# Kernel tuning notes

Hardware: AMD Instinct MI355X
Metric: run time of the kernel (lower is better)

Reference implementation:

```python
import jax, jax.numpy as jnp
import numpy as np

THRESH = 0.1        # Huber threshold (self.threshold)
CORR_WT = 1.0       # corr_wt
ENTROPY_WT = 0.0001 # entropy_wt
BS, N = 32, 1024    # n_pts = nv = 1024 hardcoded in multi_pose_with_pts


def setup_inputs() -> dict:
    key = jax.random.key(0)
    ks = jax.random.split(key, 7)
    return {
        "points_1": jax.random.normal(ks[0], (BS, N, 3), jnp.float32),
        "points_2": jax.random.normal(ks[1], (BS, N, 3), jnp.float32),
        "assign_mat_1": jax.random.normal(ks[2], (BS, N, N), jnp.float32),
        "assign_mat_2": jax.random.normal(ks[3], (BS, N, N), jnp.float32),
        "scale": jax.random.uniform(ks[4], (BS,), jnp.float32, 0.5, 1.5),
        "rotation": jax.random.normal(ks[5], (BS, 3, 3), jnp.float32),
        "translation": jax.random.normal(ks[6], (BS, 3), jnp.float32),
    }


def _transform(sRt, pts):
    # apply 4x4 pose to [b, n, 3] points (homogeneous, keep xyz)
    return jnp.einsum('bij,bnj->bni', sRt[:, :3, :3], pts) + sRt[:, :3, 3][:, None, :]


def _chamfer(x, y):
    # squared pairwise distances [b, n, m]; loss = mean min both directions
    d = (jnp.sum(x * x, -1)[:, :, None] + jnp.sum(y * y, -1)[:, None, :]
         - 2.0 * jnp.einsum('bnd,bmd->bnm', x, y))
    d = jnp.maximum(d, 0.0)
    return jnp.mean(jnp.min(d, axis=2)) + jnp.mean(jnp.min(d, axis=1))


def _corr(a, b):
    # smooth-L1-like (Huber) correspondence loss
    diff = jnp.abs(a - b)
    loss = jnp.where(diff > THRESH, diff - THRESH / 2.0, diff * diff / (2.0 * THRESH))
    return CORR_WT * jnp.mean(jnp.sum(loss, axis=2))


def _entropy(assign_mat, soft_assign, axis):
    log_assign = jax.nn.log_softmax(assign_mat, axis=axis)
    return ENTROPY_WT * jnp.mean(-jnp.sum(soft_assign * log_assign, axis=axis))


def _cos_loss(m1, m2, eps=1e-8):
    a = m1.reshape(m1.shape[0], -1)
    b = m2.reshape(m2.shape[0], -1)
    na = jnp.maximum(jnp.linalg.norm(a, axis=1), eps)
    nb = jnp.maximum(jnp.linalg.norm(b, axis=1), eps)
    return jnp.mean(1.0 - jnp.sum(a * b, axis=1) / (na * nb))


def reference(points_1, points_2, assign_mat_1, assign_mat_2, scale, rotation, translation):
    sa1 = jax.nn.softmax(assign_mat_1, axis=2)
    sa2 = jax.nn.softmax(assign_mat_2, axis=2)

    # pose_dict_RT: sRt = [[s*R, t], [0, 1]]
    sR = rotation * scale[:, None, None]
    sRt = jnp.concatenate([sR, translation[:, :, None]], axis=2)          # b 3 4
    bottom = jnp.broadcast_to(jnp.array([0., 0., 0., 1.], sRt.dtype), (sRt.shape[0], 1, 4))
    sRt12 = jnp.concatenate([sRt, bottom], axis=1)                        # b 4 4
    sRt21 = jnp.linalg.inv(sRt12)

    p1in2 = jnp.einsum('bnm,bmd->bnd', sa1, points_2)
    p2in1 = jnp.einsum('bnm,bmd->bnd', sa2, points_1)
    p1to2 = _transform(sRt12, points_1)
    p2to1 = _transform(sRt21, points_2)

    cd1 = _chamfer(p1to2, p1in2)
    cd2 = _chamfer(p2to1, p2in1)
    total = (cd1 + cd2
             + _corr(p1in2, p1to2) + _corr(p2in1, p2to1)
             + _entropy(assign_mat_1, sa1, 2) + _entropy(assign_mat_2, sa2, 2)
             + _cos_loss(assign_mat_1, assign_mat_2)
             + _entropy(assign_mat_1, sa1, 1) + _entropy(assign_mat_2, sa2, 1))
    return total
```

## Files before the change

### kernel.cpp

```cpp
#include <hip/hip_runtime.h>
#include <math.h>

#define BSZ 32
#define NP  1024

#define OFF_ACC    0
#define OFF_COS    8
#define OFF_COLC1  104
#define OFF_COLT1  (OFF_COLC1 + 32768)
#define OFF_COLC2  (OFF_COLC1 + 65536)
#define OFF_COLT2  (OFF_COLC1 + 98304)
#define ZERO_FLOATS (OFF_COLC1 + 131072)
#define OFF_MIN    ZERO_FLOATS
#define OFF_POSE   (OFF_MIN + 131072)
#define OFF_P1TO2  (OFF_POSE + 768)
#define OFF_P2TO1  (OFF_P1TO2 + 98304)
#define OFF_P1IN2  (OFF_P2TO1 + 98304)
#define OFF_P2IN1  (OFF_P1IN2 + 98304)

__global__ void k_pose(const float* __restrict__ scale,
                       const float* __restrict__ rot,
                       const float* __restrict__ tr,
                       float* __restrict__ pose) {
    int b = threadIdx.x;
    if (b >= BSZ) return;
    float s = scale[b];
    float M[9];
#pragma unroll
    for (int i = 0; i < 9; ++i) M[i] = rot[b * 9 + i] * s;
    float t0 = tr[b * 3 + 0], t1 = tr[b * 3 + 1], t2 = tr[b * 3 + 2];
    float det = M[0] * (M[4] * M[8] - M[5] * M[7])
              - M[1] * (M[3] * M[8] - M[5] * M[6])
              + M[2] * (M[3] * M[7] - M[4] * M[6]);
    float id = 1.0f / det;
    float inv[9];
    inv[0] =  (M[4] * M[8] - M[5] * M[7]) * id;
    inv[1] = -(M[1] * M[8] - M[2] * M[7]) * id;
    inv[2] =  (M[1] * M[5] - M[2] * M[4]) * id;
    inv[3] = -(M[3] * M[8] - M[5] * M[6]) * id;
    inv[4] =  (M[0] * M[8] - M[2] * M[6]) * id;
    inv[5] = -(M[0] * M[5] - M[2] * M[3]) * id;
    inv[6] =  (M[3] * M[7] - M[4] * M[6]) * id;
    inv[7] = -(M[0] * M[7] - M[1] * M[6]) * id;
    inv[8] =  (M[0] * M[4] - M[1] * M[3]) * id;
    float u0 = -(inv[0] * t0 + inv[1] * t1 + inv[2] * t2);
    float u1 = -(inv[3] * t0 + inv[4] * t1 + inv[5] * t2);
    float u2 = -(inv[6] * t0 + inv[7] * t1 + inv[8] * t2);
    float* P = pose + b * 24;
#pragma unroll
    for (int i = 0; i < 9; ++i) P[i] = M[i];
    P[9] = t0; P[10] = t1; P[11] = t2;
#pragma unroll
    for (int i = 0; i < 9; ++i) P[12 + i] = inv[i];
    P[21] = u0; P[22] = u1; P[23] = u2;
}

__global__ void k_transform(const float* __restrict__ p1, const float* __restrict__ p2,
                            const float* __restrict__ pose,
                            float* __restrict__ p1to2, float* __restrict__ p2to1) {
    int idx = blockIdx.x * 256 + threadIdx.x;
    int b = idx >> 10;
    const float* P = pose + b * 24;
    float x = p1[idx * 3 + 0], y = p1[idx * 3 + 1], z = p1[idx * 3 + 2];
    p1to2[idx * 3 + 0] = P[0] * x + P[1] * y + P[2] * z + P[9];
    p1to2[idx * 3 + 1] = P[3] * x + P[4] * y + P[5] * z + P[10];
    p1to2[idx * 3 + 2] = P[6] * x + P[7] * y + P[8] * z + P[11];
    x = p2[idx * 3 + 0]; y = p2[idx * 3 + 1]; z = p2[idx * 3 + 2];
    p2to1[idx * 3 + 0] = P[12] * x + P[13] * y + P[14] * z + P[21];
    p2to1[idx * 3 + 1] = P[15] * x + P[16] * y + P[17] * z + P[22];
    p2to1[idx * 3 + 2] = P[18] * x + P[19] * y + P[20] * z + P[23];
}

__global__ __launch_bounds__(256) void k_big(
    const float* __restrict__ am1, const float* __restrict__ am2,
    const float* __restrict__ pts1, const float* __restrict__ pts2,
    float* __restrict__ p1in2, float* __restrict__ p2in1,
    float* __restrict__ colC1, float* __restrict__ colT1,
    float* __restrict__ colC2, float* __restrict__ colT2,
    float* __restrict__ cosacc, float* __restrict__ acc) {
    const int b  = blockIdx.x >> 4;
    const int rb = blockIdx.x & 15;
    const int wv = threadIdx.x >> 6;
    const int ln = threadIdx.x & 63;
    const int row0 = rb * 64 + wv * 16;

    float pA[16][3];
    float pB[16][3];
#pragma unroll
    for (int j = 0; j < 4; ++j)
#pragma unroll
        for (int k = 0; k < 4; ++k) {
            int c = 256 * j + 4 * ln + k;
            int i = 4 * j + k;
            pA[i][0] = pts2[(b * NP + c) * 3 + 0];
            pA[i][1] = pts2[(b * NP + c) * 3 + 1];
            pA[i][2] = pts2[(b * NP + c) * 3 + 2];
            pB[i][0] = pts1[(b * NP + c) * 3 + 0];
            pB[i][1] = pts1[(b * NP + c) * 3 + 1];
            pB[i][2] = pts1[(b * NP + c) * 3 + 2];
        }

    float C1[16], T1[16], C2[16], T2[16];
#pragma unroll
    for (int i = 0; i < 16; ++i) { C1[i] = 0.f; T1[i] = 0.f; C2[i] = 0.f; T2[i] = 0.f; }
    float dacc = 0.f, n1a = 0.f, n2a = 0.f, e2a = 0.f, sSa = 0.f;

    const float4* rA = (const float4*)(am1 + ((size_t)b * NP + row0) * NP);
    const float4* rB = (const float4*)(am2 + ((size_t)b * NP + row0) * NP);

#pragma unroll 1
    for (int r = 0; r < 16; ++r) {
        float4 a[4], c4[4];
#pragma unroll
        for (int j = 0; j < 4; ++j) {
            a[j]  = rA[(size_t)r * 256 + ln + 64 * j];
            c4[j] = rB[(size_t)r * 256 + ln + 64 * j];
        }
#pragma unroll
        for (int j = 0; j < 4; ++j) {
            dacc += a[j].x * c4[j].x + a[j].y * c4[j].y + a[j].z * c4[j].z + a[j].w * c4[j].w;
            n1a  += a[j].x * a[j].x + a[j].y * a[j].y + a[j].z * a[j].z + a[j].w * a[j].w;
            n2a  += c4[j].x * c4[j].x + c4[j].y * c4[j].y + c4[j].z * c4[j].z + c4[j].w * c4[j].w;
        }
        {
            float R = 0.f, Su = 0.f, q0 = 0.f, q1 = 0.f, q2 = 0.f;
#pragma unroll
            for (int j = 0; j < 4; ++j) {
                float* e = (float*)&a[j];
#pragma unroll
                for (int k = 0; k < 4; ++k) {
                    int i = 4 * j + k;
                    float v  = e[k];
                    float ex = __expf(v);
                    R += ex; Su += ex * v;
                    q0 += ex * pA[i][0]; q1 += ex * pA[i][1]; q2 += ex * pA[i][2];
                    C1[i] += ex;
                    e[k] = ex;
                }
            }
#pragma unroll
            for (int m = 1; m < 64; m <<= 1) {
                R  += __shfl_xor(R, m);  Su += __shfl_xor(Su, m);
                q0 += __shfl_xor(q0, m); q1 += __shfl_xor(q1, m); q2 += __shfl_xor(q2, m);
            }
            float inv = 1.0f / R;
#pragma unroll
            for (int j = 0; j < 4; ++j) {
                float* e = (float*)&a[j];
#pragma unroll
                for (int k = 0; k < 4; ++k) T1[4 * j + k] += e[k] * inv;
            }
            float S = Su * inv;
            if (ln == 0) {
                e2a += __logf(R) - S;
                sSa += S;
                int row = b * NP + row0 + r;
                p1in2[row * 3 + 0] = q0 * inv;
                p1in2[row * 3 + 1] = q1 * inv;
                p1in2[row * 3 + 2] = q2 * inv;
            }
        }
        {
            float R = 0.f, Su = 0.f, q0 = 0.f, q1 = 0.f, q2 = 0.f;
#pragma unroll
            for (int j = 0; j < 4; ++j) {
                float* e = (float*)&c4[j];
#pragma unroll
                for (int k = 0; k < 4; ++k) {
                    int i = 4 * j + k;
                    float v  = e[k];
                    float ex = __expf(v);
                    R += ex; Su += ex * v;
                    q0 += ex * pB[i][0]; q1 += ex * pB[i][1]; q2 += ex * pB[i][2];
                    C2[i] += ex;
                    e[k] = ex;
                }
            }
#pragma unroll
            for (int m = 1; m < 64; m <<= 1) {
                R  += __shfl_xor(R, m);  Su += __shfl_xor(Su, m);
                q0 += __shfl_xor(q0, m); q1 += __shfl_xor(q1, m); q2 += __shfl_xor(q2, m);
            }
            float inv = 1.0f / R;
#pragma unroll
            for (int j = 0; j < 4; ++j) {
                float* e = (float*)&c4[j];
#pragma unroll
                for (int k = 0; k < 4; ++k) T2[4 * j + k] += e[k] * inv;
            }
            float S = Su * inv;
            if (ln == 0) {
                e2a += __logf(R) - S;
                sSa += S;
                int row = b * NP + row0 + r;
                p2in1[row * 3 + 0] = q0 * inv;
                p2in1[row * 3 + 1] = q1 * inv;
                p2in1[row * 3 + 2] = q2 * inv;
            }
        }
    }

#pragma unroll
    for (int j = 0; j < 4; ++j)
#pragma unroll
        for (int k = 0; k < 4; ++k) {
            int i = 4 * j + k;
            int o = b * NP + 256 * j + 4 * ln + k;
            atomicAdd(&colC1[o], C1[i]);
            atomicAdd(&colT1[o], T1[i]);
            atomicAdd(&colC2[o], C2[i]);
            atomicAdd(&colT2[o], T2[i]);
        }
#pragma unroll
    for (int m = 1; m < 64; m <<= 1) {
        dacc += __shfl_xor(dacc, m);
        n1a  += __shfl_xor(n1a, m);
        n2a  += __shfl_xor(n2a, m);
    }
    if (ln == 0) {
        atomicAdd(&cosacc[b], dacc);
        atomicAdd(&cosacc[32 + b], n1a);
        atomicAdd(&cosacc[64 + b], n2a);
        atomicAdd(&acc[0], e2a);
        atomicAdd(&acc[1], sSa);
    }
}

__global__ void k_cols(const float* __restrict__ colC1, const float* __restrict__ colT1,
                       const float* __restrict__ colC2, const float* __restrict__ colT2,
                       float* __restrict__ acc) {
    int idx = blockIdx.x * 256 + threadIdx.x;
    float v;
    if (idx < 32768) v = colT1[idx] * __logf(colC1[idx]);
    else { int i2 = idx - 32768; v = colT2[i2] * __logf(colC2[i2]); }
#pragma unroll
    for (int m = 1; m < 64; m <<= 1) v += __shfl_xor(v, m);
    if ((threadIdx.x & 63) == 0) atomicAdd(&acc[2], v);
}

__global__ __launch_bounds__(256) void k_chamfer(
    const float* __restrict__ p1to2, const float* __restrict__ p1in2,
    const float* __restrict__ p2to1, const float* __restrict__ p2in1,
    float* __restrict__ minarr) {
    int blk   = blockIdx.x;
    int chunk = blk & 3;
    int b     = (blk >> 2) & 31;
    int dir   = (blk >> 7) & 1;
    int pair  = blk >> 8;
    const float* X; const float* Y;
    if (pair == 0) { X = dir ? p1in2 : p1to2; Y = dir ? p1to2 : p1in2; }
    else           { X = dir ? p2in1 : p2to1; Y = dir ? p2to1 : p2in1; }
    __shared__ float ys[256 * 3];
    int t = threadIdx.x;
    int yi = b * NP + chunk * 256 + t;
    ys[t * 3 + 0] = Y[yi * 3 + 0];
    ys[t * 3 + 1] = Y[yi * 3 + 1];
    ys[t * 3 + 2] = Y[yi * 3 + 2];
    __syncthreads();
    float* marr = minarr + ((size_t)(pair * 2 + dir) * 32 + b) * NP;
    float x0[4], x1[4], x2[4], mn[4];
#pragma unroll
    for (int i = 0; i < 4; ++i) {
        int xi = b * NP + i * 256 + t;
        x0[i] = X[xi * 3 + 0]; x1[i] = X[xi * 3 + 1]; x2[i] = X[xi * 3 + 2];
        mn[i] = 3.0e38f;
    }
    for (int o = 0; o < 256; ++o) {
        float y0 = ys[o * 3 + 0], y1 = ys[o * 3 + 1], y2 = ys[o * 3 + 2];
#pragma unroll
        for (int i = 0; i < 4; ++i) {
            float d0 = x0[i] - y0, d1 = x1[i] - y1, d2 = x2[i] - y2;
            float d = d0 * d0 + d1 * d1 + d2 * d2;
            mn[i] = fminf(mn[i], d);
        }
    }
#pragma unroll
    for (int i = 0; i < 4; ++i)
        atomicMin((unsigned int*)&marr[i * 256 + t], __float_as_uint(mn[i]));
}

__global__ void k_corr(const float* __restrict__ p1in2, const float* __restrict__ p1to2,
                       const float* __restrict__ p2in1, const float* __restrict__ p2to1,
                       float* __restrict__ acc) {
    int idx = blockIdx.x * 256 + threadIdx.x;
    const float* A; const float* P;
    int i = idx;
    if (i < 32768) { A = p1in2; P = p1to2; }
    else           { A = p2in1; P = p2to1; i -= 32768; }
    float s = 0.f;
#pragma unroll
    for (int d = 0; d < 3; ++d) {
        float df = fabsf(A[i * 3 + d] - P[i * 3 + d]);
        s += (df > 0.1f) ? (df - 0.05f) : (df * df * 5.0f);
    }
#pragma unroll
    for (int m = 1; m < 64; m <<= 1) s += __shfl_xor(s, m);
    if ((threadIdx.x & 63) == 0) atomicAdd(&acc[3], s);
}

__global__ void k_minsum(const float* __restrict__ minarr, float* __restrict__ acc) {
    int idx = blockIdx.x * 256 + threadIdx.x;
    float v = minarr[idx];
#pragma unroll
    for (int m = 1; m < 64; m <<= 1) v += __shfl_xor(v, m);
    if ((threadIdx.x & 63) == 0) atomicAdd(&acc[4], v);
}

__global__ void k_final(const float* __restrict__ acc, const float* __restrict__ cosacc,
                        float* __restrict__ out) {
    if (threadIdx.x != 0) return;
    const float invBN = 1.0f / 32768.0f;
    float ent2 = 1e-4f * acc[0] * invBN;
    float ent1 = 1e-4f * (acc[2] - acc[1]) * invBN;
    float corr = acc[3] * invBN;
    float cham = acc[4] * invBN;
    float cosl = 0.f;
    for (int b = 0; b < 32; ++b) {
        float dot = cosacc[b];
        float na = fmaxf(sqrtf(cosacc[32 + b]), 1e-8f);
        float nb = fmaxf(sqrtf(cosacc[64 + b]), 1e-8f);
        cosl += 1.0f - dot / (na * nb);
    }
    cosl *= (1.0f / 32.0f);
    out[0] = cham + corr + ent2 + ent1 + cosl;
}

extern "C" void kernel_launch(void* const* d_in, const int* in_sizes, int n_in,
                              void* d_out, int out_size, void* d_ws, size_t ws_size,
                              hipStream_t stream) {
    const float* p1    = (const float*)d_in[0];
    const float* p2    = (const float*)d_in[1];
    const float* am1   = (const float*)d_in[2];
    const float* am2   = (const float*)d_in[3];
    const float* scale = (const float*)d_in[4];
    const float* rot   = (const float*)d_in[5];
    const float* tr    = (const float*)d_in[6];

    float* ws = (float*)d_ws;
    float* acc    = ws + OFF_ACC;
    float* cosacc = ws + OFF_COS;
    float* colC1  = ws + OFF_COLC1;
    float* colT1  = ws + OFF_COLT1;
    float* colC2  = ws + OFF_COLC2;
    float* colT2  = ws + OFF_COLT2;
    float* minarr = ws + OFF_MIN;
    float* pose   = ws + OFF_POSE;
    float* p1to2  = ws + OFF_P1TO2;
    float* p2to1  = ws + OFF_P2TO1;
    float* p1in2  = ws + OFF_P1IN2;
    float* p2in1  = ws + OFF_P2IN1;

    hipMemsetAsync(ws, 0, ZERO_FLOATS * sizeof(float), stream);
    hipMemsetAsync(minarr, 0x7F, 131072 * sizeof(float), stream);

    k_pose<<<1, 64, 0, stream>>>(scale, rot, tr, pose);
    k_transform<<<128, 256, 0, stream>>>(p1, p2, pose, p1to2, p2to1);
    k_big<<<512, 256, 0, stream>>>(am1, am2, p1, p2, p1in2, p2in1,
                                   colC1, colT1, colC2, colT2, cosacc, acc);
    k_cols<<<256, 256, 0, stream>>>(colC1, colT1, colC2, colT2, acc);
    k_chamfer<<<512, 256, 0, stream>>>(p1to2, p1in2, p2to1, p2in1, minarr);
    k_corr<<<256, 256, 0, stream>>>(p1in2, p1to2, p2in1, p2to1, acc);
    k_minsum<<<512, 256, 0, stream>>>(minarr, acc);
    k_final<<<1, 64, 0, stream>>>(acc, cosacc, (float*)d_out);
}
```

Measured before the change: 495.1 us.

## Restructure big kernel with prefetch and LDS column reduction, fuse tail kernels

The main softmax/column kernel now uses twice as many blocks with 8 rows per wave, double-buffers the assignment-matrix row loads, packs point coordinates as bf16 pairs in registers, and reduces column sums in shared memory before issuing global atomics. The chamfer kernel now loads the whole target cloud into LDS as SoA and computes the full minimum per point directly, which removes the atomicMin buffer, its memset and the separate min-sum kernel. The corr and column-entropy reductions are merged into one tail kernel. Storing points as bf16 lowers the precision of the soft-assigned point estimates, and the extra per-block shared-memory reductions add overhead.

```diff
diff --git a/kernel.cpp b/kernel.cpp
--- a/kernel.cpp
+++ b/kernel.cpp
@@ -11,12 +11,17 @@
 #define OFF_COLC2  (OFF_COLC1 + 65536)
 #define OFF_COLT2  (OFF_COLC1 + 98304)
 #define ZERO_FLOATS (OFF_COLC1 + 131072)
-#define OFF_MIN    ZERO_FLOATS
-#define OFF_POSE   (OFF_MIN + 131072)
+#define OFF_POSE   ZERO_FLOATS
 #define OFF_P1TO2  (OFF_POSE + 768)
 #define OFF_P2TO1  (OFF_P1TO2 + 98304)
 #define OFF_P1IN2  (OFF_P2TO1 + 98304)
 #define OFF_P2IN1  (OFF_P1IN2 + 98304)
+
+__device__ __forceinline__ unsigned int pkbf(float lo, float hi) {
+    return (__float_as_uint(lo) >> 16) | (__float_as_uint(hi) & 0xffff0000u);
+}
+__device__ __forceinline__ float bflo(unsigned int p) { return __uint_as_float(p << 16); }
+__device__ __forceinline__ float bfhi(unsigned int p) { return __uint_as_float(p & 0xffff0000u); }
 
 __global__ void k_pose(const float* __restrict__ scale,
                        const float* __restrict__ rot,
@@ -78,27 +83,38 @@
     float* __restrict__ colC1, float* __restrict__ colT1,
     float* __restrict__ colC2, float* __restrict__ colT2,
     float* __restrict__ cosacc, float* __restrict__ acc) {
-    const int b  = blockIdx.x >> 4;
-    const int rb = blockIdx.x & 15;
+    const int b  = blockIdx.x >> 5;
+    const int rb = blockIdx.x & 31;
     const int wv = threadIdx.x >> 6;
     const int ln = threadIdx.x & 63;
-    const int row0 = rb * 64 + wv * 16;
-
-    float pA[16][3];
-    float pB[16][3];
-#pragma unroll
-    for (int j = 0; j < 4; ++j)
-#pragma unroll
-        for (int k = 0; k < 4; ++k) {
-            int c = 256 * j + 4 * ln + k;
-            int i = 4 * j + k;
-            pA[i][0] = pts2[(b * NP + c) * 3 + 0];
-            pA[i][1] = pts2[(b * NP + c) * 3 + 1];
-            pA[i][2] = pts2[(b * NP + c) * 3 + 2];
-            pB[i][0] = pts1[(b * NP + c) * 3 + 0];
-            pB[i][1] = pts1[(b * NP + c) * 3 + 1];
-            pB[i][2] = pts1[(b * NP + c) * 3 + 2];
-        }
+    const int row0 = rb * 32 + wv * 8;
+
+    __shared__ float cacc[4][NP];
+    {
+        float* cf = (float*)cacc;
+#pragma unroll
+        for (int i = 0; i < 16; ++i) cf[threadIdx.x + 256 * i] = 0.f;
+    }
+    __syncthreads();
+
+    unsigned int pax[4][2], pay[4][2], paz[4][2];
+    unsigned int pbx[4][2], pby[4][2], pbz[4][2];
+#pragma unroll
+    for (int j = 0; j < 4; ++j) {
+        int base = (b * NP + 256 * j + 4 * ln) * 3;
+        float4 t0 = *(const float4*)(pts2 + base);
+        float4 t1 = *(const float4*)(pts2 + base + 4);
+        float4 t2 = *(const float4*)(pts2 + base + 8);
+        pax[j][0] = pkbf(t0.x, t0.w); pax[j][1] = pkbf(t1.z, t2.y);
+        pay[j][0] = pkbf(t0.y, t1.x); pay[j][1] = pkbf(t1.w, t2.z);
+        paz[j][0] = pkbf(t0.z, t1.y); paz[j][1] = pkbf(t2.x, t2.w);
+        t0 = *(const float4*)(pts1 + base);
+        t1 = *(const float4*)(pts1 + base + 4);
+        t2 = *(const float4*)(pts1 + base + 8);
+        pbx[j][0] = pkbf(t0.x, t0.w); pbx[j][1] = pkbf(t1.z, t2.y);
+        pby[j][0] = pkbf(t0.y, t1.x); pby[j][1] = pkbf(t1.w, t2.z);
+        pbz[j][0] = pkbf(t0.z, t1.y); pbz[j][1] = pkbf(t2.x, t2.w);
+    }
 
     float C1[16], T1[16], C2[16], T2[16];
 #pragma unroll
@@ -108,94 +124,111 @@
     const float4* rA = (const float4*)(am1 + ((size_t)b * NP + row0) * NP);
     const float4* rB = (const float4*)(am2 + ((size_t)b * NP + row0) * NP);
 
-#pragma unroll 1
-    for (int r = 0; r < 16; ++r) {
-        float4 a[4], c4[4];
+    float4 ab[2][4], cb[2][4];
+#pragma unroll
+    for (int j = 0; j < 4; ++j) { ab[0][j] = rA[ln + 64 * j]; cb[0][j] = rB[ln + 64 * j]; }
+
+#pragma unroll
+    for (int r = 0; r < 8; ++r) {
+        const int cu = r & 1, nx = cu ^ 1;
+        if (r < 7) {
+#pragma unroll
+            for (int j = 0; j < 4; ++j) {
+                ab[nx][j] = rA[(size_t)(r + 1) * 256 + ln + 64 * j];
+                cb[nx][j] = rB[(size_t)(r + 1) * 256 + ln + 64 * j];
+            }
+        }
 #pragma unroll
         for (int j = 0; j < 4; ++j) {
-            a[j]  = rA[(size_t)r * 256 + ln + 64 * j];
-            c4[j] = rB[(size_t)r * 256 + ln + 64 * j];
-        }
-#pragma unroll
-        for (int j = 0; j < 4; ++j) {
-            dacc += a[j].x * c4[j].x + a[j].y * c4[j].y + a[j].z * c4[j].z + a[j].w * c4[j].w;
-            n1a  += a[j].x * a[j].x + a[j].y * a[j].y + a[j].z * a[j].z + a[j].w * a[j].w;
-            n2a  += c4[j].x * c4[j].x + c4[j].y * c4[j].y + c4[j].z * c4[j].z + c4[j].w * c4[j].w;
+            float4 a = ab[cu][j], c = cb[cu][j];
+            dacc = fmaf(a.x, c.x, fmaf(a.y, c.y, fmaf(a.z, c.z, fmaf(a.w, c.w, dacc))));
+            n1a  = fmaf(a.x, a.x, fmaf(a.y, a.y, fmaf(a.z, a.z, fmaf(a.w, a.w, n1a))));
+            n2a  = fmaf(c.x, c.x, fmaf(c.y, c.y, fmaf(c.z, c.z, fmaf(c.w, c.w, n2a))));
         }
         {
-            float R = 0.f, Su = 0.f, q0 = 0.f, q1 = 0.f, q2 = 0.f;
-#pragma unroll
-            for (int j = 0; j < 4; ++j) {
-                float* e = (float*)&a[j];
-#pragma unroll
-                for (int k = 0; k < 4; ++k) {
-                    int i = 4 * j + k;
-                    float v  = e[k];
-                    float ex = __expf(v);
-                    R += ex; Su += ex * v;
-                    q0 += ex * pA[i][0]; q1 += ex * pA[i][1]; q2 += ex * pA[i][2];
-                    C1[i] += ex;
-                    e[k] = ex;
-                }
+            float R = 0.f, Su = 0.f, qx = 0.f, qy = 0.f, qz = 0.f;
+#pragma unroll
+            for (int j = 0; j < 4; ++j) {
+                float4 v = ab[cu][j];
+                float e0 = __expf(v.x), e1 = __expf(v.y), e2 = __expf(v.z), e3 = __expf(v.w);
+                R += (e0 + e1) + (e2 + e3);
+                Su = fmaf(e0, v.x, Su); Su = fmaf(e1, v.y, Su);
+                Su = fmaf(e2, v.z, Su); Su = fmaf(e3, v.w, Su);
+                qx = fmaf(e0, bflo(pax[j][0]), qx); qx = fmaf(e1, bfhi(pax[j][0]), qx);
+                qx = fmaf(e2, bflo(pax[j][1]), qx); qx = fmaf(e3, bfhi(pax[j][1]), qx);
+                qy = fmaf(e0, bflo(pay[j][0]), qy); qy = fmaf(e1, bfhi(pay[j][0]), qy);
+                qy = fmaf(e2, bflo(pay[j][1]), qy); qy = fmaf(e3, bfhi(pay[j][1]), qy);
+                qz = fmaf(e0, bflo(paz[j][0]), qz); qz = fmaf(e1, bfhi(paz[j][0]), qz);
+                qz = fmaf(e2, bflo(paz[j][1]), qz); qz = fmaf(e3, bfhi(paz[j][1]), qz);
+                C1[4 * j + 0] += e0; C1[4 * j + 1] += e1;
+                C1[4 * j + 2] += e2; C1[4 * j + 3] += e3;
+                ab[cu][j] = make_float4(e0, e1, e2, e3);
             }
 #pragma unroll
             for (int m = 1; m < 64; m <<= 1) {
                 R  += __shfl_xor(R, m);  Su += __shfl_xor(Su, m);
-                q0 += __shfl_xor(q0, m); q1 += __shfl_xor(q1, m); q2 += __shfl_xor(q2, m);
+                qx += __shfl_xor(qx, m); qy += __shfl_xor(qy, m); qz += __shfl_xor(qz, m);
             }
             float inv = 1.0f / R;
 #pragma unroll
             for (int j = 0; j < 4; ++j) {
-                float* e = (float*)&a[j];
-#pragma unroll
-                for (int k = 0; k < 4; ++k) T1[4 * j + k] += e[k] * inv;
+                float4 e = ab[cu][j];
+                T1[4 * j + 0] = fmaf(e.x, inv, T1[4 * j + 0]);
+                T1[4 * j + 1] = fmaf(e.y, inv, T1[4 * j + 1]);
+                T1[4 * j + 2] = fmaf(e.z, inv, T1[4 * j + 2]);
+                T1[4 * j + 3] = fmaf(e.w, inv, T1[4 * j + 3]);
             }
             float S = Su * inv;
             if (ln == 0) {
                 e2a += __logf(R) - S;
                 sSa += S;
                 int row = b * NP + row0 + r;
-                p1in2[row * 3 + 0] = q0 * inv;
-                p1in2[row * 3 + 1] = q1 * inv;
-                p1in2[row * 3 + 2] = q2 * inv;
+                p1in2[row * 3 + 0] = qx * inv;
+                p1in2[row * 3 + 1] = qy * inv;
+                p1in2[row * 3 + 2] = qz * inv;
             }
         }
         {
-            float R = 0.f, Su = 0.f, q0 = 0.f, q1 = 0.f, q2 = 0.f;
-#pragma unroll
-            for (int j = 0; j < 4; ++j) {
-                float* e = (float*)&c4[j];
-#pragma unroll
-                for (int k = 0; k < 4; ++k) {
-                    int i = 4 * j + k;
-                    float v  = e[k];
-                    float ex = __expf(v);
-                    R += ex; Su += ex * v;
-                    q0 += ex * pB[i][0]; q1 += ex * pB[i][1]; q2 += ex * pB[i][2];
-                    C2[i] += ex;
-                    e[k] = ex;
-                }
+            float R = 0.f, Su = 0.f, qx = 0.f, qy = 0.f, qz = 0.f;
+#pragma unroll
+            for (int j = 0; j < 4; ++j) {
+                float4 v = cb[cu][j];
+                float e0 = __expf(v.x), e1 = __expf(v.y), e2 = __expf(v.z), e3 = __expf(v.w);
+                R += (e0 + e1) + (e2 + e3);
+                Su = fmaf(e0, v.x, Su); Su = fmaf(e1, v.y, Su);
+                Su = fmaf(e2, v.z, Su); Su = fmaf(e3, v.w, Su);
+                qx = fmaf(e0, bflo(pbx[j][0]), qx); qx = fmaf(e1, bfhi(pbx[j][0]), qx);
+                qx = fmaf(e2, bflo(pbx[j][1]), qx); qx = fmaf(e3, bfhi(pbx[j][1]), qx);
+                qy = fmaf(e0, bflo(pby[j][0]), qy); qy = fmaf(e1, bfhi(pby[j][0]), qy);
+                qy = fmaf(e2, bflo(pby[j][1]), qy); qy = fmaf(e3, bfhi(pby[j][1]), qy);
+                qz = fmaf(e0, bflo(pbz[j][0]), qz); qz = fmaf(e1, bfhi(pbz[j][0]), qz);
+                qz = fmaf(e2, bflo(pbz[j][1]), qz); qz = fmaf(e3, bfhi(pbz[j][1]), qz);
+                C2[4 * j + 0] += e0; C2[4 * j + 1] += e1;
+                C2[4 * j + 2] += e2; C2[4 * j + 3] += e3;
+                cb[cu][j] = make_float4(e0, e1, e2, e3);
             }
 #pragma unroll
             for (int m = 1; m < 64; m <<= 1) {
                 R  += __shfl_xor(R, m);  Su += __shfl_xor(Su, m);
-                q0 += __shfl_xor(q0, m); q1 += __shfl_xor(q1, m); q2 += __shfl_xor(q2, m);
+                qx += __shfl_xor(qx, m); qy += __shfl_xor(qy, m); qz += __shfl_xor(qz, m);
             }
             float inv = 1.0f / R;
 #pragma unroll
             for (int j = 0; j < 4; ++j) {
-                float* e = (float*)&c4[j];
-#pragma unroll
-                for (int k = 0; k < 4; ++k) T2[4 * j + k] += e[k] * inv;
+                float4 e = cb[cu][j];
+                T2[4 * j + 0] = fmaf(e.x, inv, T2[4 * j + 0]);
+                T2[4 * j + 1] = fmaf(e.y, inv, T2[4 * j + 1]);
+                T2[4 * j + 2] = fmaf(e.z, inv, T2[4 * j + 2]);
+                T2[4 * j + 3] = fmaf(e.w, inv, T2[4 * j + 3]);
             }
             float S = Su * inv;
             if (ln == 0) {
                 e2a += __logf(R) - S;
                 sSa += S;
                 int row = b * NP + row0 + r;
-                p2in1[row * 3 + 0] = q0 * inv;
-                p2in1[row * 3 + 1] = q1 * inv;
-                p2in1[row * 3 + 2] = q2 * inv;
+                p2in1[row * 3 + 0] = qx * inv;
+                p2in1[row * 3 + 1] = qy * inv;
+                p2in1[row * 3 + 2] = qz * inv;
             }
         }
     }
@@ -205,12 +238,22 @@
 #pragma unroll
         for (int k = 0; k < 4; ++k) {
             int i = 4 * j + k;
-            int o = b * NP + 256 * j + 4 * ln + k;
-            atomicAdd(&colC1[o], C1[i]);
-            atomicAdd(&colT1[o], T1[i]);
-            atomicAdd(&colC2[o], C2[i]);
-            atomicAdd(&colT2[o], T2[i]);
-        }
+            int c = 256 * j + 4 * ln + k;
+            atomicAdd(&cacc[0][c], C1[i]);
+            atomicAdd(&cacc[1][c], T1[i]);
+            atomicAdd(&cacc[2][c], C2[i]);
+            atomicAdd(&cacc[3][c], T2[i]);
+        }
+    __syncthreads();
+#pragma unroll
+    for (int qq = 0; qq < 4; ++qq) {
+        int c = 256 * qq + threadIdx.x;
+        atomicAdd(&colC1[b * NP + c], cacc[0][c]);
+        atomicAdd(&colT1[b * NP + c], cacc[1][c]);
+        atomicAdd(&colC2[b * NP + c], cacc[2][c]);
+        atomicAdd(&colT2[b * NP + c], cacc[3][c]);
+    }
+
 #pragma unroll
     for (int m = 1; m < 64; m <<= 1) {
         dacc += __shfl_xor(dacc, m);
@@ -226,84 +269,76 @@
     }
 }
 
-__global__ void k_cols(const float* __restrict__ colC1, const float* __restrict__ colT1,
+__global__ void k_tail(const float* __restrict__ colC1, const float* __restrict__ colT1,
                        const float* __restrict__ colC2, const float* __restrict__ colT2,
+                       const float* __restrict__ p1in2, const float* __restrict__ p1to2,
+                       const float* __restrict__ p2in1, const float* __restrict__ p2to1,
                        float* __restrict__ acc) {
     int idx = blockIdx.x * 256 + threadIdx.x;
     float v;
-    if (idx < 32768) v = colT1[idx] * __logf(colC1[idx]);
-    else { int i2 = idx - 32768; v = colT2[i2] * __logf(colC2[i2]); }
-#pragma unroll
-    for (int m = 1; m < 64; m <<= 1) v += __shfl_xor(v, m);
-    if ((threadIdx.x & 63) == 0) atomicAdd(&acc[2], v);
+    int i = idx;
+    const float* A; const float* P;
+    if (idx < 32768) {
+        v = colT1[idx] * __logf(colC1[idx]);
+        A = p1in2; P = p1to2;
+    } else {
+        int i2 = idx - 32768;
+        v = colT2[i2] * __logf(colC2[i2]);
+        A = p2in1; P = p2to1; i = i2;
+    }
+    float s = 0.f;
+#pragma unroll
+    for (int d = 0; d < 3; ++d) {
+        float df = fabsf(A[i * 3 + d] - P[i * 3 + d]);
+        s += (df > 0.1f) ? (df - 0.05f) : (df * df * 5.0f);
+    }
+#pragma unroll
+    for (int m = 1; m < 64; m <<= 1) { v += __shfl_xor(v, m); s += __shfl_xor(s, m); }
+    if ((threadIdx.x & 63) == 0) { atomicAdd(&acc[2], v); atomicAdd(&acc[3], s); }
 }
 
 __global__ __launch_bounds__(256) void k_chamfer(
     const float* __restrict__ p1to2, const float* __restrict__ p1in2,
     const float* __restrict__ p2to1, const float* __restrict__ p2in1,
-    float* __restrict__ minarr) {
-    int blk   = blockIdx.x;
-    int chunk = blk & 3;
-    int b     = (blk >> 2) & 31;
-    int dir   = (blk >> 7) & 1;
-    int pair  = blk >> 8;
+    float* __restrict__ acc) {
+    int blk     = blockIdx.x;
+    int quarter = blk & 3;
+    int b       = (blk >> 2) & 31;
+    int dir     = (blk >> 7) & 1;
+    int pair    = blk >> 8;
     const float* X; const float* Y;
     if (pair == 0) { X = dir ? p1in2 : p1to2; Y = dir ? p1to2 : p1in2; }
     else           { X = dir ? p2in1 : p2to1; Y = dir ? p2to1 : p2in1; }
-    __shared__ float ys[256 * 3];
+    __shared__ float ysx[NP], ysy[NP], ysz[NP];
     int t = threadIdx.x;
-    int yi = b * NP + chunk * 256 + t;
-    ys[t * 3 + 0] = Y[yi * 3 + 0];
-    ys[t * 3 + 1] = Y[yi * 3 + 1];
-    ys[t * 3 + 2] = Y[yi * 3 + 2];
+#pragma unroll
+    for (int i = 0; i < 4; ++i) {
+        int yi = i * 256 + t;
+        int g = (b * NP + yi) * 3;
+        ysx[yi] = Y[g + 0]; ysy[yi] = Y[g + 1]; ysz[yi] = Y[g + 2];
+    }
     __syncthreads();
-    float* marr = minarr + ((size_t)(pair * 2 + dir) * 32 + b) * NP;
-    float x0[4], x1[4], x2[4], mn[4];
-#pragma unroll
-    for (int i = 0; i < 4; ++i) {
-        int xi = b * NP + i * 256 + t;
-        x0[i] = X[xi * 3 + 0]; x1[i] = X[xi * 3 + 1]; x2[i] = X[xi * 3 + 2];
-        mn[i] = 3.0e38f;
-    }
-    for (int o = 0; o < 256; ++o) {
-        float y0 = ys[o * 3 + 0], y1 = ys[o * 3 + 1], y2 = ys[o * 3 + 2];
-#pragma unroll
-        for (int i = 0; i < 4; ++i) {
-            float d0 = x0[i] - y0, d1 = x1[i] - y1, d2 = x2[i] - y2;
-            float d = d0 * d0 + d1 * d1 + d2 * d2;
-            mn[i] = fminf(mn[i], d);
-        }
-    }
-#pragma unroll
-    for (int i = 0; i < 4; ++i)
-        atomicMin((unsigned int*)&marr[i * 256 + t], __float_as_uint(mn[i]));
-}
-
-__global__ void k_corr(const float* __restrict__ p1in2, const float* __restrict__ p1to2,
-                       const float* __restrict__ p2in1, const float* __restrict__ p2to1,
-                       float* __restrict__ acc) {
-    int idx = blockIdx.x * 256 + threadIdx.x;
-    const float* A; const float* P;
-    int i = idx;
-    if (i < 32768) { A = p1in2; P = p1to2; }
-    else           { A = p2in1; P = p2to1; i -= 32768; }
-    float s = 0.f;
-#pragma unroll
-    for (int d = 0; d < 3; ++d) {
-        float df = fabsf(A[i * 3 + d] - P[i * 3 + d]);
-        s += (df > 0.1f) ? (df - 0.05f) : (df * df * 5.0f);
-    }
-#pragma unroll
-    for (int m = 1; m < 64; m <<= 1) s += __shfl_xor(s, m);
-    if ((threadIdx.x & 63) == 0) atomicAdd(&acc[3], s);
-}
-
-__global__ void k_minsum(const float* __restrict__ minarr, float* __restrict__ acc) {
-    int idx = blockIdx.x * 256 + threadIdx.x;
-    float v = minarr[idx];
-#pragma unroll
-    for (int m = 1; m < 64; m <<= 1) v += __shfl_xor(v, m);
-    if ((threadIdx.x & 63) == 0) atomicAdd(&acc[4], v);
+    int xi = b * NP + quarter * 256 + t;
+    float x0 = X[xi * 3 + 0], x1 = X[xi * 3 + 1], x2 = X[xi * 3 + 2];
+    float m0 = 3.0e38f, m1 = 3.0e38f, m2 = 3.0e38f, m3 = 3.0e38f;
+    for (int o = 0; o < NP; o += 4) {
+        float4 yx = *(const float4*)&ysx[o];
+        float4 yy = *(const float4*)&ysy[o];
+        float4 yz = *(const float4*)&ysz[o];
+        float d0, d1, d2;
+        d0 = x0 - yx.x; d1 = x1 - yy.x; d2 = x2 - yz.x;
+        m0 = fminf(m0, fmaf(d0, d0, fmaf(d1, d1, d2 * d2)));
+        d0 = x0 - yx.y; d1 = x1 - yy.y; d2 = x2 - yz.y;
+        m1 = fminf(m1, fmaf(d0, d0, fmaf(d1, d1, d2 * d2)));
+        d0 = x0 - yx.z; d1 = x1 - yy.z; d2 = x2 - yz.z;
+        m2 = fminf(m2, fmaf(d0, d0, fmaf(d1, d1, d2 * d2)));
+        d0 = x0 - yx.w; d1 = x1 - yy.w; d2 = x2 - yz.w;
+        m3 = fminf(m3, fmaf(d0, d0, fmaf(d1, d1, d2 * d2)));
+    }
+    float mn = fminf(fminf(m0, m1), fminf(m2, m3));
+#pragma unroll
+    for (int m = 1; m < 64; m <<= 1) mn += __shfl_xor(mn, m);
+    if ((t & 63) == 0) atomicAdd(&acc[4], mn);
 }
 
 __global__ void k_final(const float* __restrict__ acc, const float* __restrict__ cosacc,
@@ -343,7 +378,6 @@
     float* colT1  = ws + OFF_COLT1;
     float* colC2  = ws + OFF_COLC2;
     float* colT2  = ws + OFF_COLT2;
-    float* minarr = ws + OFF_MIN;
     float* pose   = ws + OFF_POSE;
     float* p1to2  = ws + OFF_P1TO2;
     float* p2to1  = ws + OFF_P2TO1;
@@ -351,15 +385,13 @@
     float* p2in1  = ws + OFF_P2IN1;
 
     hipMemsetAsync(ws, 0, ZERO_FLOATS * sizeof(float), stream);
-    hipMemsetAsync(minarr, 0x7F, 131072 * sizeof(float), stream);
 
     k_pose<<<1, 64, 0, stream>>>(scale, rot, tr, pose);
     k_transform<<<128, 256, 0, stream>>>(p1, p2, pose, p1to2, p2to1);
-    k_big<<<512, 256, 0, stream>>>(am1, am2, p1, p2, p1in2, p2in1,
-                                   colC1, colT1, colC2, colT2, cosacc, acc);
-    k_cols<<<256, 256, 0, stream>>>(colC1, colT1, colC2, colT2, acc);
-    k_chamfer<<<512, 256, 0, stream>>>(p1to2, p1in2, p2to1, p2in1, minarr);
-    k_corr<<<256, 256, 0, stream>>>(p1in2, p1to2, p2in1, p2to1, acc);
-    k_minsum<<<512, 256, 0, stream>>>(minarr, acc);
+    k_big<<<1024, 256, 0, stream>>>(am1, am2, p1, p2, p1in2, p2in1,
+                                    colC1, colT1, colC2, colT2, cosacc, acc);
+    k_tail<<<256, 256, 0, stream>>>(colC1, colT1, colC2, colT2,
+                                    p1in2, p1to2, p2in1, p2to1, acc);
+    k_chamfer<<<512, 256, 0, stream>>>(p1to2, p1in2, p2to1, p2in1, acc);
     k_final<<<1, 64, 0, stream>>>(acc, cosacc, (float*)d_out);
 }
```

Measured after the change: 671.3 us. +35.6%, slower.
